# Kernel optimization log

Hardware: AMD Instinct MI355X
Metric: run time of the kernel (lower is better)

Reference implementation:

```python
import jax, jax.numpy as jnp
import numpy as np

D_IN, D_ATT = 48, 8

def setup_inputs() -> dict:
    key = jax.random.key(0)
    k0, k1, k2, k3, k4 = jax.random.split(key, 5)
    N = 1048576
    x = jax.random.normal(k0, (N, D_IN), dtype=jnp.float32)
    # torch Linear weights have shape [out_features, in_features]
    Wk = jax.random.normal(k1, (D_ATT, D_IN), dtype=jnp.float32) * 0.1
    Wq = jax.random.normal(k2, (D_ATT, D_IN), dtype=jnp.float32) * 0.1
    Wv = jax.random.normal(k3, (D_ATT, D_IN), dtype=jnp.float32) * 0.1
    Wo = jax.random.normal(k4, (D_IN, D_ATT), dtype=jnp.float32) * 0.1
    return {"x": x, "Wk": Wk, "Wq": Wq, "Wv": Wv, "Wo": Wo}

def reference(x, Wk, Wq, Wv, Wo):
    # q, k, v: [N, 8]
    k = x @ Wk.T
    q = x @ Wq.T
    v = x @ Wv.T
    # attn: [8, 8] = q^T k / sqrt(8), softmax over dim=1 (columns)
    scores = (q.T @ k) / jnp.sqrt(jnp.float32(D_ATT))
    attn = jax.nn.softmax(scores, axis=1)
    # pre_output: [N, 8]; output: [N, 48]
    pre = v @ attn
    return pre @ Wo.T
```

## Files before the change

kernel.cpp:

```cpp
#include <hip/hip_runtime.h>
#include <hip/hip_bf16.h>


#define DI 48

typedef __attribute__((ext_vector_type(8))) short short8;
typedef __attribute__((ext_vector_type(4))) float f32x4;

__device__ inline unsigned int pack_bf16(float lo, float hi) {
  __hip_bfloat162 h = __float22bfloat162_rn(make_float2(lo, hi));
  return *reinterpret_cast<unsigned int*>(&h);
}

constexpr int GB1 = 1024;
constexpr int GB2 = 2048;
constexpr int SDT = 20;
constexpr int SDR = 28;
constexpr int WDW = 48 * SDT + 32 * SDR;

__global__ __launch_bounds__(256) void k_gram_v(const float* __restrict__ x,
                                                const float* __restrict__ Wv,
                                                float* __restrict__ G,
                                                __hip_bfloat16* __restrict__ v,
                                                int N) {
  __shared__ unsigned int sh[4 * WDW];
  const int tid = threadIdx.x;
  const int wave = tid >> 6, lane = tid & 63;
  unsigned int* xt = &sh[wave * WDW];
  unsigned int* xr = xt + 48 * SDT;
  const int quad = lane >> 4, m = lane & 15;

  short8 wv0 = {}, wv1 = {};
  if (m < 8) {
    const float* wrow = Wv + m * DI + 8 * quad;
    float4 c0 = *(const float4*)(wrow);
    float4 c1 = *(const float4*)(wrow + 4);
    unsigned int u0[4] = { pack_bf16(c0.x, c0.y), pack_bf16(c0.z, c0.w),
                           pack_bf16(c1.x, c1.y), pack_bf16(c1.z, c1.w) };
    wv0 = *(const short8*)u0;
    if (quad < 2) {
      float4 d0 = *(const float4*)(wrow + 32);
      float4 d1 = *(const float4*)(wrow + 36);
      unsigned int u1[4] = { pack_bf16(d0.x, d0.y), pack_bf16(d0.z, d0.w),
                             pack_bf16(d1.x, d1.y), pack_bf16(d1.z, d1.w) };
      wv1 = *(const short8*)u1;
    }
  }

  f32x4 acc[3][3] = {};

  const int rows_per_block = N / GB1;
  const int rows_per_wave = rows_per_block >> 2;
  const int ntiles = rows_per_wave >> 5;
  const long long base0 = (long long)blockIdx.x * rows_per_block + wave * rows_per_wave;

  for (int tile = 0; tile < ntiles; ++tile) {
    const long long rowt = base0 + (long long)tile * 32;
    const float* src = x + rowt * DI;
    float4 va[3], vb[3];
    int rp_[3], cg_[3];
#pragma unroll
    for (int s = 0; s < 3; ++s) {
      int task = lane + 64 * s;
      int rp = task / 12, cg = task % 12;
      rp_[s] = rp; cg_[s] = cg;
      const float4* p = (const float4*)(src + (2 * rp) * DI) + cg;
      va[s] = p[0];
      vb[s] = *(const float4*)((const float*)p + DI);
    }
#pragma unroll
    for (int s = 0; s < 3; ++s) {
      int rp = rp_[s], cg = cg_[s];
      int c0 = 4 * cg;
      xt[(c0 + 0) * SDT + rp] = pack_bf16(va[s].x, vb[s].x);
      xt[(c0 + 1) * SDT + rp] = pack_bf16(va[s].y, vb[s].y);
      xt[(c0 + 2) * SDT + rp] = pack_bf16(va[s].z, vb[s].z);
      xt[(c0 + 3) * SDT + rp] = pack_bf16(va[s].w, vb[s].w);
      unsigned int ra[2] = { pack_bf16(va[s].x, va[s].y), pack_bf16(va[s].z, va[s].w) };
      unsigned int rb[2] = { pack_bf16(vb[s].x, vb[s].y), pack_bf16(vb[s].z, vb[s].w) };
      *(uint2*)&xr[(2 * rp) * SDR + 2 * cg]     = *(const uint2*)ra;
      *(uint2*)&xr[(2 * rp + 1) * SDR + 2 * cg] = *(const uint2*)rb;
    }
    asm volatile("s_waitcnt lgkmcnt(0)" ::: "memory");
    short8 f[3];
#pragma unroll
    for (int t = 0; t < 3; ++t)
      f[t] = *(const short8*)&xt[(16 * t + m) * SDT + quad * 4];
#pragma unroll
    for (int i = 0; i < 3; ++i)
#pragma unroll
      for (int j = 0; j < 3; ++j)
        acc[i][j] = __builtin_amdgcn_mfma_f32_16x16x32_bf16(f[i], f[j], acc[i][j], 0, 0, 0);
#pragma unroll
    for (int g = 0; g < 2; ++g) {
      short8 a0 = *(const short8*)&xr[(16 * g + m) * SDR + quad * 4];
      short8 a1 = {};
      if (quad < 2) a1 = *(const short8*)&xr[(16 * g + m) * SDR + 16 + quad * 4];
      f32x4 vg = {};
      vg = __builtin_amdgcn_mfma_f32_16x16x32_bf16(a0, wv0, vg, 0, 0, 0);
      vg = __builtin_amdgcn_mfma_f32_16x16x32_bf16(a1, wv1, vg, 0, 0, 0);
      if (m < 8) {
        __hip_bfloat16* vr = v + (rowt + 16 * g + 4 * quad) * 8 + m;
#pragma unroll
        for (int r = 0; r < 4; ++r) vr[r * 8] = __float2bfloat16(vg[r]);
      }
    }
  }

  __syncthreads();
  float* red = (float*)sh;
  if (wave >= 2) {
    float* dst = red + (wave - 2) * 2304 + lane * 36;
#pragma unroll
    for (int i = 0; i < 3; ++i)
#pragma unroll
      for (int j = 0; j < 3; ++j)
#pragma unroll
        for (int r = 0; r < 4; ++r) dst[(i * 3 + j) * 4 + r] = acc[i][j][r];
  }
  __syncthreads();
  if (wave < 2) {
    const float* s2 = red + wave * 2304 + lane * 36;
#pragma unroll
    for (int i = 0; i < 3; ++i)
#pragma unroll
      for (int j = 0; j < 3; ++j)
#pragma unroll
        for (int r = 0; r < 4; ++r) acc[i][j][r] += s2[(i * 3 + j) * 4 + r];
  }
  __syncthreads();
  if (wave == 1) {
    float* dst = red + lane * 36;
#pragma unroll
    for (int i = 0; i < 3; ++i)
#pragma unroll
      for (int j = 0; j < 3; ++j)
#pragma unroll
        for (int r = 0; r < 4; ++r) dst[(i * 3 + j) * 4 + r] = acc[i][j][r];
  }
  __syncthreads();
  if (wave == 0) {
    const float* s1 = red + lane * 36;
#pragma unroll
    for (int i = 0; i < 3; ++i)
#pragma unroll
      for (int j = 0; j < 3; ++j)
#pragma unroll
        for (int r = 0; r < 4; ++r) {
          float val = acc[i][j][r] + s1[(i * 3 + j) * 4 + r];
          atomicAdd(&G[(16 * i + quad * 4 + r) * 48 + 16 * j + m], val);
        }
  }
}

__global__ void k_combine(const float* __restrict__ G,
                          const float* __restrict__ Wk,
                          const float* __restrict__ Wq,
                          const float* __restrict__ Wo,
                          __hip_bfloat16* __restrict__ Mt2) {
  __shared__ float sG[2304];
  __shared__ float sWk[384], sWq[384], sWo[384];
  __shared__ float sU[384];
  __shared__ float sA[64];
  const int t = threadIdx.x;

  for (int i = t; i < 2304; i += 256) sG[i] = G[i];
  for (int i = t; i < 384; i += 256) {
    sWk[i] = Wk[i]; sWq[i] = Wq[i]; sWo[i] = Wo[i];
  }
  __syncthreads();

  for (int e = t; e < 384; e += 256) {
    int q = e & 7, i = e >> 3;
    float s = 0.f;
#pragma unroll
    for (int j = 0; j < 48; ++j) s += sG[i * 48 + j] * sWk[q * 48 + j];
    sU[q * 48 + i] = s;
  }
  __syncthreads();

  if (t < 64) {
    int p = t >> 3;
    float s = 0.f;
#pragma unroll
    for (int i = 0; i < 48; ++i) s += sWq[p * 48 + i] * sU[(t & 7) * 48 + i];
    s *= 0.35355339059327373f;
    float mx = s;
    for (int d = 1; d < 8; d <<= 1) mx = fmaxf(mx, __shfl_xor(mx, d));
    float e = expf(s - mx);
    float den = e;
    for (int d = 1; d < 8; d <<= 1) den += __shfl_xor(den, d);
    sA[t] = e / den;
  }
  __syncthreads();

  for (int e = t; e < 384; e += 256) {
    int p = e & 7, col = e >> 3;
    float s = 0.f;
#pragma unroll
    for (int q = 0; q < 8; ++q) s += sA[p * 8 + q] * sWo[col * 8 + q];
    Mt2[col * 8 + p] = __float2bfloat16(s);
  }
}

__global__ __launch_bounds__(256) void k_out_v(const __hip_bfloat16* __restrict__ v,
                                               const __hip_bfloat16* __restrict__ Mt2,
                                               float* __restrict__ out, int N) {
  const int tid = threadIdx.x;
  const int wave = tid >> 6, lane = tid & 63;
  const int quad = lane >> 4, m = lane & 15;

  short8 b[3] = {short8{}, short8{}, short8{}};
  if (quad == 0) {
#pragma unroll
    for (int t = 0; t < 3; ++t)
      b[t] = *(const short8*)(Mt2 + (16 * t + m) * 8);
  }

  const int rows_per_block = N / GB2;
  const int rows_per_wave = rows_per_block >> 2;
  const int ng = rows_per_wave >> 4;
  const long long base = (long long)blockIdx.x * rows_per_block + wave * rows_per_wave;

  for (int g = 0; g < ng; ++g) {
    const long long rowg = base + (long long)g * 16;
    short8 af = {};
    if (quad == 0) af = *(const short8*)(v + (rowg + m) * 8);
    f32x4 acc[3] = {};
#pragma unroll
    for (int t = 0; t < 3; ++t)
      acc[t] = __builtin_amdgcn_mfma_f32_16x16x32_bf16(af, b[t], acc[t], 0, 0, 0);
    float* orow = out + rowg * DI;
#pragma unroll
    for (int t = 0; t < 3; ++t)
#pragma unroll
      for (int r = 0; r < 4; ++r)
        orow[(quad * 4 + r) * DI + 16 * t + m] = acc[t][r];
  }
}

extern "C" void kernel_launch(void* const* d_in, const int* in_sizes, int n_in,
                              void* d_out, int out_size, void* d_ws, size_t ws_size,
                              hipStream_t stream) {
  const float* x  = (const float*)d_in[0];
  const float* Wk = (const float*)d_in[1];
  const float* Wq = (const float*)d_in[2];
  const float* Wv = (const float*)d_in[3];
  const float* Wo = (const float*)d_in[4];
  float* out = (float*)d_out;
  const int N = in_sizes[0] / DI;

  float* G = (float*)d_ws;
  __hip_bfloat16* Mt2 = (__hip_bfloat16*)((char*)d_ws + 9216);
  __hip_bfloat16* v   = (__hip_bfloat16*)((char*)d_ws + 16384);

  hipMemsetAsync(G, 0, 2304 * sizeof(float), stream);
  k_gram_v<<<GB1, 256, 0, stream>>>(x, Wv, G, v, N);
  k_combine<<<1, 256, 0, stream>>>(G, Wk, Wq, Wo, Mt2);
  k_out_v<<<GB2, 256, 0, stream>>>(v, Mt2, out, N);
}
```

Measured before the change: 378.3 us.

## Double-buffer x tile loads, spread Gram atomics over copies, vectorize output stores

```diff
diff --git a/kernel.cpp b/kernel.cpp
--- a/kernel.cpp
+++ b/kernel.cpp
@@ -14,6 +14,7 @@
 
 constexpr int GB1 = 1024;
 constexpr int GB2 = 2048;
+constexpr int NC  = 32;
 constexpr int SDT = 20;
 constexpr int SDR = 28;
 constexpr int WDW = 48 * SDT + 32 * SDR;
@@ -51,26 +52,25 @@
 
   const int rows_per_block = N / GB1;
   const int rows_per_wave = rows_per_block >> 2;
-  const int ntiles = rows_per_wave >> 5;
   const long long base0 = (long long)blockIdx.x * rows_per_block + wave * rows_per_wave;
 
-  for (int tile = 0; tile < ntiles; ++tile) {
-    const long long rowt = base0 + (long long)tile * 32;
-    const float* src = x + rowt * DI;
-    float4 va[3], vb[3];
-    int rp_[3], cg_[3];
+  auto LOADT = [&](int tile, float4* va, float4* vb) {
 #pragma unroll
     for (int s = 0; s < 3; ++s) {
       int task = lane + 64 * s;
       int rp = task / 12, cg = task % 12;
-      rp_[s] = rp; cg_[s] = cg;
-      const float4* p = (const float4*)(src + (2 * rp) * DI) + cg;
+      const float4* p = (const float4*)(x + (base0 + tile * 32 + 2 * rp) * DI) + cg;
       va[s] = p[0];
       vb[s] = *(const float4*)((const float*)p + DI);
     }
+  };
+
+  auto PROCESS = [&](int tile, const float4* va, const float4* vb) {
+    const long long rowt = base0 + (long long)tile * 32;
 #pragma unroll
     for (int s = 0; s < 3; ++s) {
-      int rp = rp_[s], cg = cg_[s];
+      int task = lane + 64 * s;
+      int rp = task / 12, cg = task % 12;
       int c0 = 4 * cg;
       xt[(c0 + 0) * SDT + rp] = pack_bf16(va[s].x, vb[s].x);
       xt[(c0 + 1) * SDT + rp] = pack_bf16(va[s].y, vb[s].y);
@@ -105,6 +105,16 @@
         for (int r = 0; r < 4; ++r) vr[r * 8] = __float2bfloat16(vg[r]);
       }
     }
+  };
+
+  float4 vaA[3], vbA[3], vaB[3], vbB[3];
+  LOADT(0, vaA, vbA);
+#pragma unroll
+  for (int t = 0; t < 8; t += 2) {
+    if (t + 1 < 8) LOADT(t + 1, vaB, vbB);
+    PROCESS(t, vaA, vbA);
+    if (t + 2 < 8) LOADT(t + 2, vaA, vbA);
+    if (t + 1 < 8) PROCESS(t + 1, vaB, vbB);
   }
 
   __syncthreads();
@@ -141,6 +151,7 @@
   __syncthreads();
   if (wave == 0) {
     const float* s1 = red + lane * 36;
+    float* Gp = G + (blockIdx.x & (NC - 1)) * 2304;
 #pragma unroll
     for (int i = 0; i < 3; ++i)
 #pragma unroll
@@ -148,7 +159,7 @@
 #pragma unroll
         for (int r = 0; r < 4; ++r) {
           float val = acc[i][j][r] + s1[(i * 3 + j) * 4 + r];
-          atomicAdd(&G[(16 * i + quad * 4 + r) * 48 + 16 * j + m], val);
+          atomicAdd(&Gp[(16 * i + quad * 4 + r) * 48 + 16 * j + m], val);
         }
   }
 }
@@ -164,7 +175,12 @@
   __shared__ float sA[64];
   const int t = threadIdx.x;
 
-  for (int i = t; i < 2304; i += 256) sG[i] = G[i];
+  for (int i = t; i < 2304; i += 256) {
+    float s = 0.f;
+#pragma unroll
+    for (int c = 0; c < NC; ++c) s += G[c * 2304 + i];
+    sG[i] = s;
+  }
   for (int i = t; i < 384; i += 256) {
     sWk[i] = Wk[i]; sWq[i] = Wq[i]; sWo[i] = Wo[i];
   }
@@ -229,13 +245,11 @@
     f32x4 acc[3] = {};
 #pragma unroll
     for (int t = 0; t < 3; ++t)
-      acc[t] = __builtin_amdgcn_mfma_f32_16x16x32_bf16(af, b[t], acc[t], 0, 0, 0);
+      acc[t] = __builtin_amdgcn_mfma_f32_16x16x32_bf16(b[t], af, acc[t], 0, 0, 0);
     float* orow = out + rowg * DI;
 #pragma unroll
     for (int t = 0; t < 3; ++t)
-#pragma unroll
-      for (int r = 0; r < 4; ++r)
-        orow[(quad * 4 + r) * DI + 16 * t + m] = acc[t][r];
+      *(float4*)(orow + m * DI + 16 * t + 4 * quad) = *(const float4*)&acc[t];
   }
 }
 
@@ -251,10 +265,10 @@
   const int N = in_sizes[0] / DI;
 
   float* G = (float*)d_ws;
-  __hip_bfloat16* Mt2 = (__hip_bfloat16*)((char*)d_ws + 9216);
-  __hip_bfloat16* v   = (__hip_bfloat16*)((char*)d_ws + 16384);
-
-  hipMemsetAsync(G, 0, 2304 * sizeof(float), stream);
+  __hip_bfloat16* Mt2 = (__hip_bfloat16*)((char*)d_ws + 294912);
+  __hip_bfloat16* v   = (__hip_bfloat16*)((char*)d_ws + 307200);
+
+  hipMemsetAsync(G, 0, NC * 2304 * sizeof(float), stream);
   k_gram_v<<<GB1, 256, 0, stream>>>(x, Wv, G, v, N);
   k_combine<<<1, 256, 0, stream>>>(G, Wk, Wq, Wo, Mt2);
   k_out_v<<<GB2, 256, 0, stream>>>(v, Mt2, out, N);
```

After: 384.4 us. About the same (+1.6%).
